# Kernel optimization log

Measured on AMD Instinct MI355X. Metric: run time of the kernel, lower is better.

The kernel has to match this reference:

```python
import jax, jax.numpy as jnp
import numpy as np

D, S, E, MPE = 256, 128, 512, 4096
B, N = 2, 4096


def _rope(x):
    # x: (..., n, d); RoPE over axis -2 positions (dim=1 in the torch code)
    n, d = x.shape[-2], x.shape[-1]
    half = d // 2
    pos = jnp.arange(n, dtype=x.dtype)
    inv_freq = 10000.0 ** (-jnp.arange(half, dtype=x.dtype) / half)
    sinusoid = pos[:, None] * inv_freq  # (n, half)
    sin, cos = jnp.sin(sinusoid), jnp.cos(sinusoid)
    x1, x2 = jnp.split(x, 2, axis=-1)
    return jnp.concatenate([x1 * cos - x2 * sin, x2 * cos + x1 * sin], axis=-1)


def setup_inputs() -> dict:
    key = jax.random.key(0)
    ks = jax.random.split(key, 12)
    std = 0.02
    return {
        "query": jax.random.normal(ks[0], (B, N, D), jnp.float32),
        "ln_w": jnp.ones((D,), jnp.float32),
        "ln_b": jnp.zeros((D,), jnp.float32),
        "Wu": jax.random.normal(ks[1], (D, E), jnp.float32) / np.float32(np.sqrt(D)),
        "bu": jnp.zeros((E,), jnp.float32),
        "Wv": jax.random.normal(ks[2], (D, E), jnp.float32) / np.float32(np.sqrt(D)),
        "bv": jnp.zeros((E,), jnp.float32),
        "Wbase": jax.random.normal(ks[3], (D, S), jnp.float32) / np.float32(np.sqrt(D)),
        "bbase": jnp.zeros((S,), jnp.float32),
        "q_w": jax.random.normal(ks[4], (1, S), jnp.float32) * std,
        "q_b": jnp.zeros((1, S), jnp.float32),
        "k_w": jax.random.normal(ks[5], (1, S), jnp.float32) * std,
        "k_b": jnp.zeros((1, S), jnp.float32),
        "w_rel": jax.random.normal(ks[6], (2 * MPE - 1,), jnp.float32) * std,
        "Wo": jax.random.normal(ks[7], (E, D), jnp.float32) / np.float32(np.sqrt(E)),
        "bo": jnp.zeros((D,), jnp.float32),
    }


def reference(query, ln_w, ln_b, Wu, bu, Wv, bv, Wbase, bbase,
              q_w, q_b, k_w, k_b, w_rel, Wo, bo):
    mpe = (w_rel.shape[0] + 1) // 2
    bsz, n, d = query.shape
    # LayerNorm
    mu = query.mean(axis=-1, keepdims=True)
    var = ((query - mu) ** 2).mean(axis=-1, keepdims=True)
    x = (query - mu) * jax.lax.rsqrt(var + 1e-5) * ln_w + ln_b
    # gated projections
    u = jax.nn.silu(x @ Wu + bu)       # (B,N,E)
    v = jax.nn.silu(x @ Wv + bv)       # (B,N,E)
    base = jax.nn.silu(x @ Wbase + bbase)  # (B,N,S)
    q = _rope(base * q_w + q_b)
    k = _rope(base * k_w + k_b)
    qk = jnp.einsum('bms,bns->bmn', q, k)  # (B,N,N)
    # Toeplitz relative-position bias: bias[i,j] = w_rel[mpe-1 + j - i]
    # (equivalent to the torch pad/repeat/reshape construction, sliced to n)
    i = jnp.arange(n)
    bias = w_rel[(mpe - 1) + i[None, :] - i[:, None]]  # (N,N)
    kernel = jnp.square(jax.nn.relu(qk / mpe + bias))
    out = (u * jnp.einsum('bmn,bne->bme', kernel, v)) @ Wo + bo
    return out
```

## Files before the change

kernel.cpp:

```cpp
#include <hip/hip_runtime.h>
#include <hip/hip_bf16.h>
#include <math.h>

typedef __bf16 bf16_8 __attribute__((ext_vector_type(8)));
typedef float f32x4 __attribute__((ext_vector_type(4)));

#define D_ 256
#define S_ 128
#define E_ 512
#define MPE_ 4096
#define B_ 2
#define N_ 4096
#define M_TOT (B_*N_)

__device__ __forceinline__ ushort f2b(float f) {
  union { float f; uint u; } x; x.f = f;
  uint r = (x.u + 0x7FFFu + ((x.u >> 16) & 1u)) >> 16;
  return (ushort)r;
}
__device__ __forceinline__ float b2f(ushort b) {
  union { uint u; float f; } x; x.u = ((uint)b) << 16;
  return x.f;
}

__device__ __forceinline__ void gl_lds16(const void* g, void* l) {
  __builtin_amdgcn_global_load_lds(
      (const __attribute__((address_space(1))) void*)g,
      (__attribute__((address_space(3))) void*)l, 16, 0, 0);
}

__global__ __launch_bounds__(256) void ln_kernel(const float* __restrict__ q,
    const float* __restrict__ w, const float* __restrict__ b,
    ushort* __restrict__ x) {
  int wid = threadIdx.x >> 6, lane = threadIdx.x & 63;
  int row = blockIdx.x * 4 + wid;
  const float* qr = q + (size_t)row * D_;
  float4 v = *(const float4*)(qr + lane * 4);
  float s  = v.x + v.y + v.z + v.w;
  float ss = v.x*v.x + v.y*v.y + v.z*v.z + v.w*v.w;
  #pragma unroll
  for (int off = 32; off; off >>= 1) {
    s  += __shfl_xor(s, off);
    ss += __shfl_xor(ss, off);
  }
  float mu   = s * (1.0f / 256.0f);
  float var  = ss * (1.0f / 256.0f) - mu * mu;
  float rstd = rsqrtf(var + 1e-5f);
  ushort4 o;
  float vv[4] = {v.x, v.y, v.z, v.w};
  ushort ot[4];
  #pragma unroll
  for (int j = 0; j < 4; ++j) {
    int c = lane * 4 + j;
    ot[j] = f2b((vv[j] - mu) * rstd * w[c] + b[c]);
  }
  o.x = ot[0]; o.y = ot[1]; o.z = ot[2]; o.w = ot[3];
  *(ushort4*)(x + (size_t)row * D_ + lane * 4) = o;
}

__global__ void wt_kernel(const float* __restrict__ in, ushort* __restrict__ out,
                          int R, int C) {
  int o = blockIdx.x * 256 + threadIdx.x;
  if (o >= R * C) return;
  int c = o / R, r = o - c * R;
  out[o] = f2b(in[r * C + c]);
}

template<int EPI>
__global__ __launch_bounds__(256) void gemm_kernel(
    const ushort* __restrict__ A, const ushort* __restrict__ Bt,
    const float* __restrict__ bias, void* __restrict__ out,
    int M, int N, int K) {
  __shared__ alignas(16) ushort As[128 * 64];
  __shared__ alignas(16) ushort Bs[64 * 64];
  int tid = threadIdx.x;
  int lane = tid & 63, wid = tid >> 6;
  int m0 = blockIdx.x * 128, n0 = blockIdx.y * 64;
  int r16 = lane & 15, kq = lane >> 4;
  f32x4 acc[2][4] = {};
  for (int k0 = 0; k0 < K; k0 += 64) {
    __syncthreads();
    #pragma unroll
    for (int t = 0; t < 4; ++t) {
      int cid = tid + t * 256;
      int row = cid >> 3, c = cid & 7;
      uint4 d = *(const uint4*)(A + ((size_t)(m0 + row) * K + k0 + c * 8));
      *(uint4*)&As[row * 64 + ((c ^ (row & 7)) * 8)] = d;
    }
    #pragma unroll
    for (int t = 0; t < 2; ++t) {
      int cid = tid + t * 256;
      int row = cid >> 3, c = cid & 7;
      uint4 d = *(const uint4*)(Bt + ((size_t)(n0 + row) * K + k0 + c * 8));
      *(uint4*)&Bs[row * 64 + ((c ^ (row & 7)) * 8)] = d;
    }
    __syncthreads();
    #pragma unroll
    for (int ks = 0; ks < 2; ++ks) {
      bf16_8 af[2], bfr[4];
      int c = ks * 4 + kq;
      #pragma unroll
      for (int fm = 0; fm < 2; ++fm) {
        int r = wid * 32 + fm * 16 + r16;
        af[fm] = *(const bf16_8*)&As[r * 64 + ((c ^ (r & 7)) * 8)];
      }
      #pragma unroll
      for (int fn = 0; fn < 4; ++fn) {
        int r = fn * 16 + r16;
        bfr[fn] = *(const bf16_8*)&Bs[r * 64 + ((c ^ (r & 7)) * 8)];
      }
      #pragma unroll
      for (int fm = 0; fm < 2; ++fm)
        #pragma unroll
        for (int fn = 0; fn < 4; ++fn)
          acc[fm][fn] = __builtin_amdgcn_mfma_f32_16x16x32_bf16(af[fm], bfr[fn], acc[fm][fn], 0, 0, 0);
    }
  }
  #pragma unroll
  for (int fm = 0; fm < 2; ++fm)
    #pragma unroll
    for (int fn = 0; fn < 4; ++fn)
      #pragma unroll
      for (int reg = 0; reg < 4; ++reg) {
        int ml = wid * 32 + fm * 16 + kq * 4 + reg;
        int nl = fn * 16 + r16;
        size_t gm = m0 + ml, gn = n0 + nl;
        float val = acc[fm][fn][reg] + bias[gn];
        if (EPI == 0) {
          float y = val / (1.0f + expf(-val));
          ((ushort*)out)[gm * N + gn] = f2b(y);
        } else if (EPI == 2) {
          float y = val / (1.0f + expf(-val));
          ((ushort*)out)[gn * (size_t)M_TOT + gm] = f2b(y);
        } else {
          ((float*)out)[gm * N + gn] = val;
        }
      }
}

__global__ __launch_bounds__(256) void rope_kernel(const ushort* __restrict__ base,
    const float* __restrict__ qw, const float* __restrict__ qb,
    const float* __restrict__ kw, const float* __restrict__ kb,
    ushort* __restrict__ Q, ushort* __restrict__ Kk) {
  int g = blockIdx.x * 256 + threadIdx.x;
  int row = g >> 6, i = g & 63;
  int n = row & (N_ - 1);
  float invf = powf(10000.0f, -(float)i * (1.0f / 64.0f));
  float sv, cv;
  sincosf((float)n * invf, &sv, &cv);
  const float sc = 0.015625f;
  float b1 = b2f(base[row * S_ + i]), b2 = b2f(base[row * S_ + 64 + i]);
  float x1q = b1 * qw[i] + qb[i], x2q = b2 * qw[64 + i] + qb[64 + i];
  Q[row * S_ + i]      = f2b((x1q * cv - x2q * sv) * sc);
  Q[row * S_ + 64 + i] = f2b((x2q * cv + x1q * sv) * sc);
  float x1k = b1 * kw[i] + kb[i], x2k = b2 * kw[64 + i] + kb[64 + i];
  Kk[row * S_ + i]      = f2b((x1k * cv - x2k * sv) * sc);
  Kk[row * S_ + 64 + i] = f2b((x2k * cv + x1k * sv) * sc);
}

__global__ __launch_bounds__(256, 2) void attn_kernel(
    const ushort* __restrict__ Q, const ushort* __restrict__ Kd,
    const ushort* __restrict__ VT, const ushort* __restrict__ U,
    const float* __restrict__ w_rel, ushort* __restrict__ KVU) {
  __shared__ alignas(16) ushort Ks[2][64 * 128];
  __shared__ alignas(16) ushort Vs[2][128 * 64];
  __shared__ alignas(16) ushort Pb[2][32 * 64];
  __shared__ float WrL[2][128];
  const int tid = threadIdx.x, lane = tid & 63, wid = tid >> 6;
  const int b = blockIdx.z, m0 = blockIdx.x * 64, e0 = blockIdx.y * 128;
  const int r16 = lane & 15, kq = lane >> 4;
  const int wm = wid >> 1, wl = wid & 1;

  bf16_8 qf[2][4];
  #pragma unroll
  for (int fm = 0; fm < 2; ++fm)
    #pragma unroll
    for (int ks = 0; ks < 4; ++ks)
      qf[fm][ks] = *(const bf16_8*)(Q +
          ((size_t)(b * N_ + m0 + wm * 32 + fm * 16 + r16) * S_ + ks * 32 + kq * 8));

  auto stage_kv = [&](int bi, int t) {
    int n0s = t * 64;
    #pragma unroll
    for (int tt = 0; tt < 4; ++tt) {
      int p = tt * 256 + wid * 64 + lane;
      int row = p >> 4, sc2 = p & 15;
      int cc = sc2 ^ (row & 7);
      gl_lds16(Kd + ((size_t)(b * N_ + n0s + row) * S_ + cc * 8),
               &Ks[bi][(tt * 256 + wid * 64) * 8]);
    }
    #pragma unroll
    for (int tt = 0; tt < 4; ++tt) {
      int p = tt * 256 + wid * 64 + lane;
      int er = p >> 3, sc2 = p & 7;
      int nc = sc2 ^ (er & 7);
      gl_lds16(VT + ((size_t)(e0 + er) * M_TOT + b * N_ + n0s + nc * 8),
               &Vs[bi][(tt * 256 + wid * 64) * 8]);
    }
  };

  f32x4 pv[2][4] = {};

  stage_kv(0, 0);
  if (tid < 127) WrL[0][tid] = w_rel[4032 - m0 + tid];
  asm volatile("s_waitcnt vmcnt(0) lgkmcnt(0)" ::: "memory");
  __builtin_amdgcn_s_barrier();

  auto body = [&](int CUR, int t) {
    float wv = 0.f;
    bool hw = (t < 63) && (tid < 127);
    if (hw) wv = w_rel[4032 + (t + 1) * 64 - m0 + tid];
    if (t < 63) stage_kv(CUR ^ 1, t + 1);
    const ushort* ksb = Ks[CUR];
    f32x4 sacc[2][2] = {};
    __builtin_amdgcn_s_setprio(1);
    #pragma unroll
    for (int ks = 0; ks < 4; ++ks) {
      bf16_8 kf[2];
      #pragma unroll
      for (int fn = 0; fn < 2; ++fn) {
        int r = wl * 32 + fn * 16 + r16;
        int c = ks * 4 + kq;
        kf[fn] = *(const bf16_8*)&ksb[r * 128 + ((c ^ (r & 7)) * 8)];
      }
      #pragma unroll
      for (int fm = 0; fm < 2; ++fm)
        #pragma unroll
        for (int fn = 0; fn < 2; ++fn)
          sacc[fm][fn] = __builtin_amdgcn_mfma_f32_16x16x32_bf16(qf[fm][ks], kf[fn], sacc[fm][fn], 0, 0, 0);
    }
    __builtin_amdgcn_s_setprio(0);
    if (hw) WrL[CUR ^ 1][tid] = wv;
    char* psb = (char*)&Pb[wm][0];
    #pragma unroll
    for (int fm = 0; fm < 2; ++fm)
      #pragma unroll
      for (int fn = 0; fn < 2; ++fn)
        #pragma unroll
        for (int reg = 0; reg < 4; ++reg) {
          int ml = fm * 16 + kq * 4 + reg;
          int nl = wl * 32 + fn * 16 + r16;
          float tv = sacc[fm][fn][reg] + WrL[CUR][63 + nl - wm * 32 - ml];
          tv = fmaxf(tv, 0.0f);
          *(ushort*)(psb + ((ml * 128 + nl * 2) ^ ((ml & 7) << 4))) = f2b(tv * tv);
        }
    asm volatile("s_waitcnt lgkmcnt(0)" ::: "memory");
    __builtin_amdgcn_s_barrier();
    const ushort* vsb = Vs[CUR];
    __builtin_amdgcn_s_setprio(1);
    #pragma unroll
    for (int ks = 0; ks < 2; ++ks) {
      bf16_8 pa[2];
      #pragma unroll
      for (int fm = 0; fm < 2; ++fm) {
        int r = fm * 16 + r16;
        pa[fm] = *(const bf16_8*)(psb + ((r * 128 + ks * 64 + kq * 16) ^ ((r & 7) << 4)));
      }
      #pragma unroll
      for (int fe = 0; fe < 4; ++fe) {
        int rv = wl * 64 + fe * 16 + r16;
        int cv = ks * 4 + kq;
        bf16_8 vf = *(const bf16_8*)&vsb[rv * 64 + ((cv ^ (rv & 7)) * 8)];
        #pragma unroll
        for (int fm = 0; fm < 2; ++fm)
          pv[fm][fe] = __builtin_amdgcn_mfma_f32_16x16x32_bf16(pa[fm], vf, pv[fm][fe], 0, 0, 0);
      }
    }
    __builtin_amdgcn_s_setprio(0);
    asm volatile("s_waitcnt vmcnt(0) lgkmcnt(0)" ::: "memory");
    __builtin_amdgcn_s_barrier();
  };

  for (int t2 = 0; t2 < 32; ++t2) {
    body(0, 2 * t2);
    body(1, 2 * t2 + 1);
  }

  #pragma unroll
  for (int fm = 0; fm < 2; ++fm)
    #pragma unroll
    for (int fe = 0; fe < 4; ++fe)
      #pragma unroll
      for (int reg = 0; reg < 4; ++reg) {
        int ml = fm * 16 + kq * 4 + reg;
        size_t grow = (size_t)b * N_ + m0 + wm * 32 + ml;
        size_t ge = e0 + wl * 64 + fe * 16 + r16;
        float uu = b2f(U[grow * E_ + ge]);
        KVU[grow * E_ + ge] = f2b(uu * pv[fm][fe][reg]);
      }
}

extern "C" void kernel_launch(void* const* d_in, const int* in_sizes, int n_in,
                              void* d_out, int out_size, void* d_ws, size_t ws_size,
                              hipStream_t stream) {
  const float* query = (const float*)d_in[0];
  const float* ln_w  = (const float*)d_in[1];
  const float* ln_b  = (const float*)d_in[2];
  const float* Wu    = (const float*)d_in[3];
  const float* bu    = (const float*)d_in[4];
  const float* Wv    = (const float*)d_in[5];
  const float* bv    = (const float*)d_in[6];
  const float* Wbase = (const float*)d_in[7];
  const float* bbase = (const float*)d_in[8];
  const float* q_w   = (const float*)d_in[9];
  const float* q_b   = (const float*)d_in[10];
  const float* k_w   = (const float*)d_in[11];
  const float* k_b   = (const float*)d_in[12];
  const float* w_rel = (const float*)d_in[13];
  const float* Wo    = (const float*)d_in[14];
  const float* bo    = (const float*)d_in[15];
  float* out = (float*)d_out;

  char* ws = (char*)d_ws;
  ushort* X    = (ushort*)(ws);
  ushort* U    = (ushort*)(ws + (4u  << 20));
  ushort* VT   = (ushort*)(ws + (12u << 20));
  ushort* BASE = (ushort*)(ws + (20u << 20));
  ushort* Qb   = (ushort*)(ws + (22u << 20));
  ushort* Kb   = (ushort*)(ws + (24u << 20));
  ushort* KVU  = (ushort*)(ws + (26u << 20));
  ushort* WUT  = (ushort*)(ws + (34u << 20));
  ushort* WVT  = (ushort*)(ws + (34u << 20) + 512*256*2);
  ushort* WBT  = (ushort*)(ws + (34u << 20) + 2*512*256*2);
  ushort* WOT  = (ushort*)(ws + (34u << 20) + 2*512*256*2 + 128*256*2);

  ln_kernel<<<2048, 256, 0, stream>>>(query, ln_w, ln_b, X);
  wt_kernel<<<(512*256 + 255) / 256, 256, 0, stream>>>(Wu, WUT, 256, 512);
  wt_kernel<<<(512*256 + 255) / 256, 256, 0, stream>>>(Wv, WVT, 256, 512);
  wt_kernel<<<(128*256 + 255) / 256, 256, 0, stream>>>(Wbase, WBT, 256, 128);
  wt_kernel<<<(512*256 + 255) / 256, 256, 0, stream>>>(Wo, WOT, 512, 256);
  gemm_kernel<0><<<dim3(64, 8), 256, 0, stream>>>(X, WUT, bu, U, 8192, 512, 256);
  gemm_kernel<2><<<dim3(64, 8), 256, 0, stream>>>(X, WVT, bv, VT, 8192, 512, 256);
  gemm_kernel<0><<<dim3(64, 2), 256, 0, stream>>>(X, WBT, bbase, BASE, 8192, 128, 256);
  rope_kernel<<<2048, 256, 0, stream>>>(BASE, q_w, q_b, k_w, k_b, Qb, Kb);
  attn_kernel<<<dim3(64, 4, 2), 256, 0, stream>>>(Qb, Kb, VT, U, w_rel, KVU);
  gemm_kernel<1><<<dim3(64, 4), 256, 0, stream>>>(KVU, WOT, bo, out, 8192, 256, 512);
}
```

Measured before the change: 157.8 us.

## Transpose score MFMA and vectorize bias loads and packed bf16 P stores

Swaps the MFMA operands so each lane holds four consecutive key columns for one query row. This lets the relative-position bias be read as one aligned float4 from four shifted copies of the bias window, and the squared-ReLU results be packed with v_cvt_pk_bf16_f32 into one 8-byte LDS store. It replaces 16 scalar LDS bias reads, software bf16 rounding and 16 scalar ushort stores per tile. In exchange it adds more LDS bias staging (four shifted copies written per tile) and a clamped index on the w_rel load.

```diff
diff --git a/kernel.cpp b/kernel.cpp
--- a/kernel.cpp
+++ b/kernel.cpp
@@ -165,11 +165,12 @@
   __shared__ alignas(16) ushort Ks[2][64 * 128];
   __shared__ alignas(16) ushort Vs[2][128 * 64];
   __shared__ alignas(16) ushort Pb[2][32 * 64];
-  __shared__ float WrL[2][128];
+  __shared__ alignas(16) float WrLc[2][4][132];
   const int tid = threadIdx.x, lane = tid & 63, wid = tid >> 6;
   const int b = blockIdx.z, m0 = blockIdx.x * 64, e0 = blockIdx.y * 128;
   const int r16 = lane & 15, kq = lane >> 4;
   const int wm = wid >> 1, wl = wid & 1;
+  const int jw = tid & 127, cpair = tid >> 7;
 
   bf16_8 qf[2][4];
   #pragma unroll
@@ -199,17 +200,29 @@
     }
   };
 
+  auto wr_load = [&](int t) -> float {
+    int idx = 4032 + t * 64 - m0 + jw;
+    if (idx > 8190) idx = 8190;
+    return w_rel[idx];
+  };
+  auto wr_store = [&](int bi, float v) {
+    WrLc[bi][cpair][jw + cpair] = v;
+    WrLc[bi][cpair + 2][jw + cpair + 2] = v;
+  };
+
   f32x4 pv[2][4] = {};
 
   stage_kv(0, 0);
-  if (tid < 127) WrL[0][tid] = w_rel[4032 - m0 + tid];
+  wr_store(0, wr_load(0));
   asm volatile("s_waitcnt vmcnt(0) lgkmcnt(0)" ::: "memory");
   __builtin_amdgcn_s_barrier();
 
+  const int csel = (r16 + 1) & 3;
+  const int abase = 63 + (wl - wm) * 32 + 4 * kq - r16 + csel;
+
   auto body = [&](int CUR, int t) {
     float wv = 0.f;
-    bool hw = (t < 63) && (tid < 127);
-    if (hw) wv = w_rel[4032 + (t + 1) * 64 - m0 + tid];
+    if (t < 63) wv = wr_load(t + 1);
     if (t < 63) stage_kv(CUR ^ 1, t + 1);
     const ushort* ksb = Ks[CUR];
     f32x4 sacc[2][2] = {};
@@ -227,23 +240,30 @@
       for (int fm = 0; fm < 2; ++fm)
         #pragma unroll
         for (int fn = 0; fn < 2; ++fn)
-          sacc[fm][fn] = __builtin_amdgcn_mfma_f32_16x16x32_bf16(qf[fm][ks], kf[fn], sacc[fm][fn], 0, 0, 0);
+          sacc[fm][fn] = __builtin_amdgcn_mfma_f32_16x16x32_bf16(kf[fn], qf[fm][ks], sacc[fm][fn], 0, 0, 0);
     }
     __builtin_amdgcn_s_setprio(0);
-    if (hw) WrL[CUR ^ 1][tid] = wv;
+    if (t < 63) wr_store(CUR ^ 1, wv);
     char* psb = (char*)&Pb[wm][0];
     #pragma unroll
     for (int fm = 0; fm < 2; ++fm)
       #pragma unroll
-      for (int fn = 0; fn < 2; ++fn)
-        #pragma unroll
-        for (int reg = 0; reg < 4; ++reg) {
-          int ml = fm * 16 + kq * 4 + reg;
-          int nl = wl * 32 + fn * 16 + r16;
-          float tv = sacc[fm][fn][reg] + WrL[CUR][63 + nl - wm * 32 - ml];
-          tv = fmaxf(tv, 0.0f);
-          *(ushort*)(psb + ((ml * 128 + nl * 2) ^ ((ml & 7) << 4))) = f2b(tv * tv);
-        }
+      for (int fn = 0; fn < 2; ++fn) {
+        int a = abase + fn * 16 - fm * 16;
+        float4 b4 = *(const float4*)&WrLc[CUR][csel][a];
+        float t0 = fmaxf(sacc[fm][fn][0] + b4.x, 0.f);
+        float t1 = fmaxf(sacc[fm][fn][1] + b4.y, 0.f);
+        float t2 = fmaxf(sacc[fm][fn][2] + b4.z, 0.f);
+        float t3 = fmaxf(sacc[fm][fn][3] + b4.w, 0.f);
+        t0 *= t0; t1 *= t1; t2 *= t2; t3 *= t3;
+        uint p01, p23;
+        asm("v_cvt_pk_bf16_f32 %0, %1, %2" : "=v"(p01) : "v"(t0), "v"(t1));
+        asm("v_cvt_pk_bf16_f32 %0, %1, %2" : "=v"(p23) : "v"(t2), "v"(t3));
+        int mp = fm * 16 + r16;
+        int nb2 = wl * 64 + fn * 32 + kq * 8;
+        uint2 pk; pk.x = p01; pk.y = p23;
+        *(uint2*)(psb + ((mp * 128 + nb2) ^ ((mp & 7) << 4))) = pk;
+      }
     asm volatile("s_waitcnt lgkmcnt(0)" ::: "memory");
     __builtin_amdgcn_s_barrier();
     const ushort* vsb = Vs[CUR];
```

After: 159.6 us. About the same (+1.1%).

## Enlarge attention block to 128 query rows with 8 waves and transposed QK MFMA

Applied to the files above, without the earlier changes.

The attention kernel now processes 128 query rows per block with 512 threads, so each staged K/V tile in shared memory is reused by twice as many rows, halving global K/V traffic. The QK product is computed transposed (K as A operand), which lets each lane gather four consecutive bias values with one float4 read from a per-lane-shifted Toeplitz bias table and pack results with v_cvt_pk_bf16_f32. The grid halves to 256 blocks, which reduces parallelism and raises per-block register and LDS pressure.

```diff
diff --git a/kernel.cpp b/kernel.cpp
--- a/kernel.cpp
+++ b/kernel.cpp
@@ -158,92 +158,115 @@
   Kk[row * S_ + 64 + i] = f2b((x2k * cv + x1k * sv) * sc);
 }
 
-__global__ __launch_bounds__(256, 2) void attn_kernel(
+__global__ __launch_bounds__(512, 2) void attn_kernel(
     const ushort* __restrict__ Q, const ushort* __restrict__ Kd,
     const ushort* __restrict__ VT, const ushort* __restrict__ U,
     const float* __restrict__ w_rel, ushort* __restrict__ KVU) {
   __shared__ alignas(16) ushort Ks[2][64 * 128];
   __shared__ alignas(16) ushort Vs[2][128 * 64];
-  __shared__ alignas(16) ushort Pb[2][32 * 64];
-  __shared__ float WrL[2][128];
+  __shared__ alignas(16) ushort Pb[128 * 64];
+  __shared__ alignas(16) float WrLc[2][4][200];
   const int tid = threadIdx.x, lane = tid & 63, wid = tid >> 6;
-  const int b = blockIdx.z, m0 = blockIdx.x * 64, e0 = blockIdx.y * 128;
+  const int b = blockIdx.z, m0 = blockIdx.x * 128, e0 = blockIdx.y * 128;
   const int r16 = lane & 15, kq = lane >> 4;
-  const int wm = wid >> 1, wl = wid & 1;
-
-  bf16_8 qf[2][4];
-  #pragma unroll
-  for (int fm = 0; fm < 2; ++fm)
+  const int wqm = wid >> 2, wqn = wid & 3;
+  const int wpm = wid >> 1, wpe = wid & 1;
+
+  bf16_8 qf[4][4];
+  #pragma unroll
+  for (int fm = 0; fm < 4; ++fm)
     #pragma unroll
     for (int ks = 0; ks < 4; ++ks)
       qf[fm][ks] = *(const bf16_8*)(Q +
-          ((size_t)(b * N_ + m0 + wm * 32 + fm * 16 + r16) * S_ + ks * 32 + kq * 8));
+          ((size_t)(b * N_ + m0 + wqm * 64 + fm * 16 + r16) * S_ + ks * 32 + kq * 8));
 
   auto stage_kv = [&](int bi, int t) {
     int n0s = t * 64;
     #pragma unroll
-    for (int tt = 0; tt < 4; ++tt) {
-      int p = tt * 256 + wid * 64 + lane;
+    for (int tt = 0; tt < 2; ++tt) {
+      int p = tt * 512 + tid;
       int row = p >> 4, sc2 = p & 15;
       int cc = sc2 ^ (row & 7);
       gl_lds16(Kd + ((size_t)(b * N_ + n0s + row) * S_ + cc * 8),
-               &Ks[bi][(tt * 256 + wid * 64) * 8]);
-    }
-    #pragma unroll
-    for (int tt = 0; tt < 4; ++tt) {
-      int p = tt * 256 + wid * 64 + lane;
+               &Ks[bi][(tt * 512 + wid * 64) * 8]);
+    }
+    #pragma unroll
+    for (int tt = 0; tt < 2; ++tt) {
+      int p = tt * 512 + tid;
       int er = p >> 3, sc2 = p & 7;
       int nc = sc2 ^ (er & 7);
       gl_lds16(VT + ((size_t)(e0 + er) * M_TOT + b * N_ + n0s + nc * 8),
-               &Vs[bi][(tt * 256 + wid * 64) * 8]);
+               &Vs[bi][(tt * 512 + wid * 64) * 8]);
     }
   };
 
+  const int bi0 = tid, bi1 = tid + 512;
+  const int bc0 = bi0 / 200, bx0 = bi0 - bc0 * 200;
+  const int bc1 = bi1 / 200, bx1 = bi1 - bc1 * 200;
+  const bool bp1 = bi1 < 800;
+  auto wr_load = [&](int t, float& w0, float& w1) {
+    int W0 = 3968 + t * 64 - m0;
+    int i0 = W0 + bx0 - 1 - bc0;
+    i0 = i0 < 0 ? 0 : (i0 > 8190 ? 8190 : i0);
+    w0 = w_rel[i0];
+    int i1 = W0 + bx1 - 1 - bc1;
+    i1 = i1 < 0 ? 0 : (i1 > 8190 ? 8190 : i1);
+    w1 = bp1 ? w_rel[i1] : 0.f;
+  };
+  auto wr_store = [&](int bi, float w0, float w1) {
+    WrLc[bi][bc0][bx0] = w0;
+    if (bp1) WrLc[bi][bc1][bx1] = w1;
+  };
+
   f32x4 pv[2][4] = {};
 
-  stage_kv(0, 0);
-  if (tid < 127) WrL[0][tid] = w_rel[4032 - m0 + tid];
+  {
+    float w0, w1;
+    wr_load(0, w0, w1);
+    stage_kv(0, 0);
+    wr_store(0, w0, w1);
+  }
   asm volatile("s_waitcnt vmcnt(0) lgkmcnt(0)" ::: "memory");
   __builtin_amdgcn_s_barrier();
 
+  const int csel = r16 & 3;
+  const int abase = 128 + 4 * kq + 16 * wqn - 64 * wqm - r16 + csel;
+
   auto body = [&](int CUR, int t) {
-    float wv = 0.f;
-    bool hw = (t < 63) && (tid < 127);
-    if (hw) wv = w_rel[4032 + (t + 1) * 64 - m0 + tid];
+    float w0 = 0.f, w1 = 0.f;
+    if (t < 63) wr_load(t + 1, w0, w1);
     if (t < 63) stage_kv(CUR ^ 1, t + 1);
     const ushort* ksb = Ks[CUR];
-    f32x4 sacc[2][2] = {};
+    f32x4 sacc[4] = {};
     __builtin_amdgcn_s_setprio(1);
     #pragma unroll
     for (int ks = 0; ks < 4; ++ks) {
-      bf16_8 kf[2];
-      #pragma unroll
-      for (int fn = 0; fn < 2; ++fn) {
-        int r = wl * 32 + fn * 16 + r16;
-        int c = ks * 4 + kq;
-        kf[fn] = *(const bf16_8*)&ksb[r * 128 + ((c ^ (r & 7)) * 8)];
-      }
-      #pragma unroll
-      for (int fm = 0; fm < 2; ++fm)
-        #pragma unroll
-        for (int fn = 0; fn < 2; ++fn)
-          sacc[fm][fn] = __builtin_amdgcn_mfma_f32_16x16x32_bf16(qf[fm][ks], kf[fn], sacc[fm][fn], 0, 0, 0);
+      int r = wqn * 16 + r16;
+      int c = ks * 4 + kq;
+      bf16_8 kf = *(const bf16_8*)&ksb[r * 128 + ((c ^ (r & 7)) * 8)];
+      #pragma unroll
+      for (int fm = 0; fm < 4; ++fm)
+        sacc[fm] = __builtin_amdgcn_mfma_f32_16x16x32_bf16(kf, qf[fm][ks], sacc[fm], 0, 0, 0);
     }
     __builtin_amdgcn_s_setprio(0);
-    if (hw) WrL[CUR ^ 1][tid] = wv;
-    char* psb = (char*)&Pb[wm][0];
-    #pragma unroll
-    for (int fm = 0; fm < 2; ++fm)
-      #pragma unroll
-      for (int fn = 0; fn < 2; ++fn)
-        #pragma unroll
-        for (int reg = 0; reg < 4; ++reg) {
-          int ml = fm * 16 + kq * 4 + reg;
-          int nl = wl * 32 + fn * 16 + r16;
-          float tv = sacc[fm][fn][reg] + WrL[CUR][63 + nl - wm * 32 - ml];
-          tv = fmaxf(tv, 0.0f);
-          *(ushort*)(psb + ((ml * 128 + nl * 2) ^ ((ml & 7) << 4))) = f2b(tv * tv);
-        }
+    if (t < 63) wr_store(CUR ^ 1, w0, w1);
+    char* psb = (char*)&Pb[0];
+    #pragma unroll
+    for (int fm = 0; fm < 4; ++fm) {
+      float4 b4 = *(const float4*)&WrLc[CUR][csel][abase - fm * 16];
+      float t0 = fmaxf(sacc[fm][0] + b4.x, 0.f);
+      float t1 = fmaxf(sacc[fm][1] + b4.y, 0.f);
+      float t2 = fmaxf(sacc[fm][2] + b4.z, 0.f);
+      float t3 = fmaxf(sacc[fm][3] + b4.w, 0.f);
+      t0 *= t0; t1 *= t1; t2 *= t2; t3 *= t3;
+      uint p01, p23;
+      asm("v_cvt_pk_bf16_f32 %0, %1, %2" : "=v"(p01) : "v"(t0), "v"(t1));
+      asm("v_cvt_pk_bf16_f32 %0, %1, %2" : "=v"(p23) : "v"(t2), "v"(t3));
+      int mp = wqm * 64 + fm * 16 + r16;
+      int nb2 = wqn * 32 + kq * 8;
+      uint2 pk; pk.x = p01; pk.y = p23;
+      *(uint2*)(psb + ((mp * 128 + nb2) ^ ((mp & 7) << 4))) = pk;
+    }
     asm volatile("s_waitcnt lgkmcnt(0)" ::: "memory");
     __builtin_amdgcn_s_barrier();
     const ushort* vsb = Vs[CUR];
@@ -253,12 +276,12 @@
       bf16_8 pa[2];
       #pragma unroll
       for (int fm = 0; fm < 2; ++fm) {
-        int r = fm * 16 + r16;
+        int r = wpm * 32 + fm * 16 + r16;
         pa[fm] = *(const bf16_8*)(psb + ((r * 128 + ks * 64 + kq * 16) ^ ((r & 7) << 4)));
       }
       #pragma unroll
       for (int fe = 0; fe < 4; ++fe) {
-        int rv = wl * 64 + fe * 16 + r16;
+        int rv = wpe * 64 + fe * 16 + r16;
         int cv = ks * 4 + kq;
         bf16_8 vf = *(const bf16_8*)&vsb[rv * 64 + ((cv ^ (rv & 7)) * 8)];
         #pragma unroll
@@ -282,9 +305,9 @@
     for (int fe = 0; fe < 4; ++fe)
       #pragma unroll
       for (int reg = 0; reg < 4; ++reg) {
-        int ml = fm * 16 + kq * 4 + reg;
-        size_t grow = (size_t)b * N_ + m0 + wm * 32 + ml;
-        size_t ge = e0 + wl * 64 + fe * 16 + r16;
+        int ml = wpm * 32 + fm * 16 + kq * 4 + reg;
+        size_t grow = (size_t)b * N_ + m0 + ml;
+        size_t ge = e0 + wpe * 64 + fe * 16 + r16;
         float uu = b2f(U[grow * E_ + ge]);
         KVU[grow * E_ + ge] = f2b(uu * pv[fm][fe][reg]);
       }
@@ -333,6 +356,6 @@
   gemm_kernel<2><<<dim3(64, 8), 256, 0, stream>>>(X, WVT, bv, VT, 8192, 512, 256);
   gemm_kernel<0><<<dim3(64, 2), 256, 0, stream>>>(X, WBT, bbase, BASE, 8192, 128, 256);
   rope_kernel<<<2048, 256, 0, stream>>>(BASE, q_w, q_b, k_w, k_b, Qb, Kb);
-  attn_kernel<<<dim3(64, 4, 2), 256, 0, stream>>>(Qb, Kb, VT, U, w_rel, KVU);
+  attn_kernel<<<dim3(32, 4, 2), 512, 0, stream>>>(Qb, Kb, VT, U, w_rel, KVU);
   gemm_kernel<1><<<dim3(64, 4), 256, 0, stream>>>(KVU, WOT, bo, out, 8192, 256, 512);
 }
```

Result: no change. 159.3 us (+1.0%).
